# Optimization experiments

Hardware: AMD Instinct MI355X
Metric: run time of the kernel (lower is better)

The kernel has to match this reference:

```python
import jax, jax.numpy as jnp
import numpy as np

B, L, D, E, He = 8, 512, 300, 64, 64  # batch, seq_len, hidden_dim, edge_embed_dim, edge_hidden_dim


def setup_inputs() -> dict:
    key = jax.random.key(0)
    ks = jax.random.split(key, 7)
    return {
        "x": jax.random.normal(ks[0], (B, L, D), jnp.float32),
        "adj": jax.random.randint(ks[1], (B, L, L), 0, 2).astype(jnp.int32),
        "edge_embedding": jax.random.normal(ks[2], (B, L, L, E), jnp.float32),
        # learned params (xavier-ish scaling)
        "W_map": jax.random.normal(ks[3], (E, He), jnp.float32) / np.sqrt(E).astype(np.float32),
        "w_ew": jax.random.normal(ks[4], (He, 1), jnp.float32) / np.sqrt(He).astype(np.float32),
        "W_eto": jax.random.normal(ks[5], (D, D), jnp.float32) / np.sqrt(D).astype(np.float32),
        "b_eto": jnp.zeros((D,), jnp.float32),
    }


def reference(x, adj, edge_embedding, W_map, w_ew, W_eto, b_eto):
    # edge_mapping -> relu (dropout is identity in eval mode)
    em = jax.nn.relu(jnp.einsum('bije,eh->bijh', edge_embedding, W_map))  # [B,L,L,He]
    # edge_weight_liner (bias-free) -> [B,L,L]
    ew = jnp.einsum('bijh,ho->bij', em, w_ew)
    # row-wise abs-mean normalization (torch: mean(dim=-1).unsqueeze(-1), + 1e-10)
    row_mean = jnp.abs(jnp.mean(ew, axis=-1, keepdims=True)) + 1e-10
    ew = ew / row_mean
    # adjacency-masked softmax (torch uses -9e15 fill)
    scores = jnp.where(adj != 0, ew, jnp.float32(-9e15))
    att = jax.nn.softmax(scores, axis=-1)  # [B,L,L]
    # dense aggregation: edge_to(input) then attention matmul, relu
    h = x @ W_eto + b_eto  # [B,L,D]
    h_edge = jax.nn.relu(jnp.einsum('bij,bjd->bid', att, h))  # [B,L,D]
    return h_edge, att
```

## Files before the change

### kernel.cpp

```cpp
#include <hip/hip_runtime.h>
#include <hip/hip_bf16.h>

#define LSEQ 512
#define DDIM 300

typedef __attribute__((ext_vector_type(8))) short short8;
typedef __attribute__((ext_vector_type(4))) float f32x4;

__device__ __forceinline__ void split4(f32x4 v, short8& hi, short8& lo, int base) {
  #pragma unroll
  for (int e = 0; e < 4; ++e) {
    const float f = v[e];
    const unsigned b = __float_as_uint(f);
    const float hf = __uint_as_float(b & 0xffff0000u);
    hi[base + e] = (short)(b >> 16);
    lo[base + e] = (short)(__float_as_uint(f - hf) >> 16);
  }
}

__global__ __launch_bounds__(256, 3) void k_fused1(
    const float* __restrict__ emb, const int* __restrict__ adj,
    const float* __restrict__ Wmap, const float* __restrict__ wew,
    const float* __restrict__ x, const float* __restrict__ Weto,
    const float* __restrict__ beto,
    float* __restrict__ att, float* __restrict__ h) {
  __shared__ float stg[2][4][1024];
  __shared__ float ew_lds[LSEQ];
  __shared__ float redA[4], redB[4], redC[4];
  const int tid = threadIdx.x;
  const int lane = tid & 63, wid = tid >> 6;
  const int c = lane & 15, g = lane >> 4;

  if (blockIdx.x >= 4096) {
    const int gt = (blockIdx.x - 4096) * 4 + wid;
    const int rt = gt / 19, dt = gt % 19;
    const int r0 = rt * 16, d0 = dt * 16;
    const int dc = min(d0 + c, DDIM - 1);
    const float* xr = x + (size_t)(r0 + c) * DDIM;

    f32x4 acc = {0.f, 0.f, 0.f, 0.f};
    #pragma unroll 3
    for (int ks = 0; ks < 9; ++ks) {
      const int k0 = ks * 32 + 8 * g;
      const f32x4 a0 = *(const f32x4*)(xr + k0);
      const f32x4 a1 = *(const f32x4*)(xr + k0 + 4);
      short8 ahi, alo;
      split4(a0, ahi, alo, 0);
      split4(a1, ahi, alo, 4);
      const float* wp = Weto + (size_t)k0 * DDIM + dc;
      const f32x4 b0 = {wp[0], wp[DDIM], wp[2 * DDIM], wp[3 * DDIM]};
      const f32x4 b1 = {wp[4 * DDIM], wp[5 * DDIM], wp[6 * DDIM], wp[7 * DDIM]};
      short8 bhi, blo;
      split4(b0, bhi, blo, 0);
      split4(b1, bhi, blo, 4);
      acc = __builtin_amdgcn_mfma_f32_16x16x32_bf16(ahi, bhi, acc, 0, 0, 0);
      acc = __builtin_amdgcn_mfma_f32_16x16x32_bf16(ahi, blo, acc, 0, 0, 0);
      acc = __builtin_amdgcn_mfma_f32_16x16x32_bf16(alo, bhi, acc, 0, 0, 0);
    }
    {
      float av[8], bv[8];
      #pragma unroll
      for (int e = 0; e < 8; ++e) {
        const int kk = 288 + 8 * g + e;
        const bool ok = kk < DDIM;
        av[e] = ok ? xr[kk] : 0.f;
        bv[e] = ok ? Weto[(size_t)kk * DDIM + dc] : 0.f;
      }
      const f32x4 a0 = {av[0], av[1], av[2], av[3]};
      const f32x4 a1 = {av[4], av[5], av[6], av[7]};
      const f32x4 b0 = {bv[0], bv[1], bv[2], bv[3]};
      const f32x4 b1 = {bv[4], bv[5], bv[6], bv[7]};
      short8 ahi, alo, bhi, blo;
      split4(a0, ahi, alo, 0);
      split4(a1, ahi, alo, 4);
      split4(b0, bhi, blo, 0);
      split4(b1, bhi, blo, 4);
      acc = __builtin_amdgcn_mfma_f32_16x16x32_bf16(ahi, bhi, acc, 0, 0, 0);
      acc = __builtin_amdgcn_mfma_f32_16x16x32_bf16(ahi, blo, acc, 0, 0, 0);
      acc = __builtin_amdgcn_mfma_f32_16x16x32_bf16(alo, bhi, acc, 0, 0, 0);
    }
    if (d0 + c < DDIM) {
      const float bb = beto[d0 + c];
      #pragma unroll
      for (int reg = 0; reg < 4; ++reg)
        h[(size_t)(r0 + 4 * g + reg) * DDIM + d0 + c] = acc[reg] + bb;
    }
    return;
  }

  short8 whi[4][2], wlo[4][2];
  #pragma unroll
  for (int nt = 0; nt < 4; ++nt) {
    #pragma unroll
    for (int s = 0; s < 2; ++s) {
      #pragma unroll
      for (int e2 = 0; e2 < 2; ++e2) {
        f32x4 w;
        #pragma unroll
        for (int e = 0; e < 4; ++e)
          w[e] = Wmap[(32 * s + 8 * g + 4 * e2 + e) * 64 + 16 * nt + c];
        split4(w, whi[nt][s], wlo[nt][s], 4 * e2);
      }
    }
  }
  float wv2[4][4];
  #pragma unroll
  for (int nt = 0; nt < 4; ++nt)
    #pragma unroll
    for (int reg = 0; reg < 4; ++reg)
      wv2[nt][reg] = wew[16 * nt + 4 * g + reg];

  const size_t rowbase = (size_t)blockIdx.x * LSEQ;
  const size_t ebase = rowbase + (size_t)wid * 128;
  const float* gbase = emb + (ebase << 6);

  float* const lb0 = &stg[0][wid][0];
  float* const lb1 = &stg[1][wid][0];

  int wwb[4];
  #pragma unroll
  for (int i = 0; i < 4; ++i)
    wwb[i] = ((i * 1024 + lane * 16) ^ ((((i & 1) * 4 + g) & 7) << 4)) >> 2;

  const int rw0 = (c * 256 + (((2 * g + 0) ^ (c & 7)) << 4)) >> 2;
  const int rw1 = (c * 256 + (((2 * g + 1) ^ (c & 7)) << 4)) >> 2;
  const int rw2 = (c * 256 + (((2 * g + 8) ^ (c & 7)) << 4)) >> 2;
  const int rw3 = (c * 256 + (((2 * g + 9) ^ (c & 7)) << 4)) >> 2;

  f32x4 q0 = *(const f32x4*)(gbase + 0 * 256 + lane * 4);
  f32x4 q1 = *(const f32x4*)(gbase + 1 * 256 + lane * 4);
  f32x4 q2 = *(const f32x4*)(gbase + 2 * 256 + lane * 4);
  f32x4 q3 = *(const f32x4*)(gbase + 3 * 256 + lane * 4);
  *(f32x4*)(lb0 + wwb[0]) = q0;
  *(f32x4*)(lb0 + wwb[1]) = q1;
  *(f32x4*)(lb0 + wwb[2]) = q2;
  *(f32x4*)(lb0 + wwb[3]) = q3;

  #pragma unroll 1
  for (int it = 0; it < 8; ++it) {
    if (it < 7) {
      const float* nt_ = gbase + (size_t)(it + 1) * 1024;
      q0 = *(const f32x4*)(nt_ + 0 * 256 + lane * 4);
      q1 = *(const f32x4*)(nt_ + 1 * 256 + lane * 4);
      q2 = *(const f32x4*)(nt_ + 2 * 256 + lane * 4);
      q3 = *(const f32x4*)(nt_ + 3 * 256 + lane * 4);
    }
    float* const rb = (it & 1) ? lb1 : lb0;
    const f32x4 a0 = *(const f32x4*)(rb + rw0);
    const f32x4 a1 = *(const f32x4*)(rb + rw1);
    const f32x4 a2 = *(const f32x4*)(rb + rw2);
    const f32x4 a3 = *(const f32x4*)(rb + rw3);

    short8 ehi[2], elo[2];
    split4(a0, ehi[0], elo[0], 0);
    split4(a1, ehi[0], elo[0], 4);
    split4(a2, ehi[1], elo[1], 0);
    split4(a3, ehi[1], elo[1], 4);

    f32x4 acc[4];
    #pragma unroll
    for (int nt = 0; nt < 4; ++nt) acc[nt] = (f32x4){0.f, 0.f, 0.f, 0.f};
    #pragma unroll
    for (int s = 0; s < 2; ++s) {
      #pragma unroll
      for (int nt = 0; nt < 4; ++nt) {
        acc[nt] = __builtin_amdgcn_mfma_f32_16x16x32_bf16(whi[nt][s], ehi[s], acc[nt], 0, 0, 0);
        acc[nt] = __builtin_amdgcn_mfma_f32_16x16x32_bf16(whi[nt][s], elo[s], acc[nt], 0, 0, 0);
        acc[nt] = __builtin_amdgcn_mfma_f32_16x16x32_bf16(wlo[nt][s], ehi[s], acc[nt], 0, 0, 0);
      }
    }
    float p = 0.f;
    #pragma unroll
    for (int nt = 0; nt < 4; ++nt)
      #pragma unroll
      for (int reg = 0; reg < 4; ++reg)
        p = fmaf(fmaxf(acc[nt][reg], 0.f), wv2[nt][reg], p);
    p += __shfl_xor(p, 16, 64);
    p += __shfl_xor(p, 32, 64);
    if (lane < 16) ew_lds[wid * 128 + it * 16 + c] = p;

    if (it < 7) {
      float* const wb = (it & 1) ? lb0 : lb1;
      *(f32x4*)(wb + wwb[0]) = q0;
      *(f32x4*)(wb + wwb[1]) = q1;
      *(f32x4*)(wb + wwb[2]) = q2;
      *(f32x4*)(wb + wwb[3]) = q3;
    }
  }
  __syncthreads();

  const float ew0 = ew_lds[tid];
  const float ew1 = ew_lds[tid + 256];

  float ls = ew0 + ew1;
  #pragma unroll
  for (int m = 32; m >= 1; m >>= 1) ls += __shfl_xor(ls, m, 64);
  if (lane == 0) redA[wid] = ls;
  __syncthreads();
  const float rmean =
      fabsf((redA[0] + redA[1] + redA[2] + redA[3]) * (1.0f / 512.0f)) + 1e-10f;

  const int a0i = adj[rowbase + tid];
  const int a1i = adj[rowbase + tid + 256];
  const float sc0 = a0i ? (ew0 / rmean) : -9e15f;
  const float sc1 = a1i ? (ew1 / rmean) : -9e15f;

  float lm = fmaxf(sc0, sc1);
  #pragma unroll
  for (int m = 32; m >= 1; m >>= 1) lm = fmaxf(lm, __shfl_xor(lm, m, 64));
  if (lane == 0) redB[wid] = lm;
  __syncthreads();
  const float mx = fmaxf(fmaxf(redB[0], redB[1]), fmaxf(redB[2], redB[3]));

  const float e0 = expf(sc0 - mx);
  const float e1 = expf(sc1 - mx);
  float es = e0 + e1;
  #pragma unroll
  for (int m = 32; m >= 1; m >>= 1) es += __shfl_xor(es, m, 64);
  if (lane == 0) redC[wid] = es;
  __syncthreads();
  const float denom = redC[0] + redC[1] + redC[2] + redC[3];

  att[rowbase + tid] = e0 / denom;
  att[rowbase + tid + 256] = e1 / denom;
}

__global__ __launch_bounds__(256) void k_out(
    const float* __restrict__ att, const float* __restrict__ h,
    float* __restrict__ out) {
  const int tid = threadIdx.x;
  const int lane = tid & 63, wid = tid >> 6;
  const int c = lane & 15, g = lane >> 4;
  const int gt = blockIdx.x * 4 + wid;
  const int b = gt / 304, rem = gt % 304;
  const int i2 = rem / 19, dt = rem % 19;
  const int i0 = i2 * 32, d0 = dt * 16;
  const int dc = min(d0 + c, DDIM - 1);
  const float* attR0 = att + ((size_t)b * LSEQ + i0 + c) * LSEQ + 8 * g;
  const float* attR1 = attR0 + (size_t)16 * LSEQ;
  const float* hB = h + (size_t)b * LSEQ * DDIM;

  f32x4 acc0 = {0.f, 0.f, 0.f, 0.f};
  f32x4 acc1 = {0.f, 0.f, 0.f, 0.f};
  #pragma unroll 2
  for (int ks = 0; ks < 16; ++ks) {
    const int k0 = ks * 32;
    const f32x4 a0 = *(const f32x4*)(attR0 + k0);
    const f32x4 a1 = *(const f32x4*)(attR0 + k0 + 4);
    const f32x4 a2 = *(const f32x4*)(attR1 + k0);
    const f32x4 a3 = *(const f32x4*)(attR1 + k0 + 4);
    short8 ahi0, alo0, ahi1, alo1;
    split4(a0, ahi0, alo0, 0);
    split4(a1, ahi0, alo0, 4);
    split4(a2, ahi1, alo1, 0);
    split4(a3, ahi1, alo1, 4);
    const float* hp = hB + (size_t)(k0 + 8 * g) * DDIM + dc;
    const f32x4 b0 = {hp[0], hp[DDIM], hp[2 * DDIM], hp[3 * DDIM]};
    const f32x4 b1 = {hp[4 * DDIM], hp[5 * DDIM], hp[6 * DDIM], hp[7 * DDIM]};
    short8 bhi, blo;
    split4(b0, bhi, blo, 0);
    split4(b1, bhi, blo, 4);
    acc0 = __builtin_amdgcn_mfma_f32_16x16x32_bf16(ahi0, bhi, acc0, 0, 0, 0);
    acc0 = __builtin_amdgcn_mfma_f32_16x16x32_bf16(ahi0, blo, acc0, 0, 0, 0);
    acc0 = __builtin_amdgcn_mfma_f32_16x16x32_bf16(alo0, bhi, acc0, 0, 0, 0);
    acc1 = __builtin_amdgcn_mfma_f32_16x16x32_bf16(ahi1, bhi, acc1, 0, 0, 0);
    acc1 = __builtin_amdgcn_mfma_f32_16x16x32_bf16(ahi1, blo, acc1, 0, 0, 0);
    acc1 = __builtin_amdgcn_mfma_f32_16x16x32_bf16(alo1, bhi, acc1, 0, 0, 0);
  }
  if (d0 + c < DDIM) {
    #pragma unroll
    for (int reg = 0; reg < 4; ++reg) {
      out[((size_t)b * LSEQ + i0 + 4 * g + reg) * DDIM + d0 + c] =
          fmaxf(acc0[reg], 0.f);
      out[((size_t)b * LSEQ + i0 + 16 + 4 * g + reg) * DDIM + d0 + c] =
          fmaxf(acc1[reg], 0.f);
    }
  }
}

extern "C" void kernel_launch(void* const* d_in, const int* in_sizes, int n_in,
                              void* d_out, int out_size, void* d_ws, size_t ws_size,
                              hipStream_t stream) {
  const float* x    = (const float*)d_in[0];
  const int*   adj  = (const int*)d_in[1];
  const float* emb  = (const float*)d_in[2];
  const float* Wmap = (const float*)d_in[3];
  const float* wew  = (const float*)d_in[4];
  const float* Weto = (const float*)d_in[5];
  const float* beto = (const float*)d_in[6];

  float* out    = (float*)d_out;
  float* h_edge = out;
  float* att    = out + (size_t)8 * LSEQ * DDIM;
  float* h      = (float*)d_ws;

  k_fused1<<<dim3(4096 + 1216), 256, 0, stream>>>(emb, adj, Wmap, wew, x, Weto,
                                                  beto, att, h);
  k_out<<<dim3(608), 256, 0, stream>>>(att, h, h_edge);
}
```

Baseline: 145.5 us.

## Store h transposed and pre-split into packed bf16 hi/lo for k_out

The projection stage now writes h as a transposed [B, D_pad, L] array of packed bf16 hi/lo pairs instead of row-major fp32. k_out can then load its B operand with contiguous 16-byte vector loads and skip the per-iteration fp32-to-bf16 split. The goal is to replace the strided scalar gathers across rows of h and to avoid repeating the split work that every attention tile did before. In exchange, the h writes in the first kernel become strided across d, and padded columns are stored as zeros.

```diff
diff --git a/kernel.cpp b/kernel.cpp
--- a/kernel.cpp
+++ b/kernel.cpp
@@ -3,9 +3,11 @@
 
 #define LSEQ 512
 #define DDIM 300
+#define DPAD 304
 
 typedef __attribute__((ext_vector_type(8))) short short8;
 typedef __attribute__((ext_vector_type(4))) float f32x4;
+typedef __attribute__((ext_vector_type(4))) unsigned u32x4;
 
 __device__ __forceinline__ void split4(f32x4 v, short8& hi, short8& lo, int base) {
   #pragma unroll
@@ -18,12 +20,20 @@
   }
 }
 
+__device__ __forceinline__ unsigned pack_split(float f) {
+  const unsigned b = __float_as_uint(f);
+  const float hf = __uint_as_float(b & 0xffff0000u);
+  const unsigned hi = b >> 16;
+  const unsigned lo = __float_as_uint(f - hf) >> 16;
+  return (hi & 0xffffu) | (lo << 16);
+}
+
 __global__ __launch_bounds__(256, 3) void k_fused1(
     const float* __restrict__ emb, const int* __restrict__ adj,
     const float* __restrict__ Wmap, const float* __restrict__ wew,
     const float* __restrict__ x, const float* __restrict__ Weto,
     const float* __restrict__ beto,
-    float* __restrict__ att, float* __restrict__ h) {
+    float* __restrict__ att, unsigned* __restrict__ hs) {
   __shared__ float stg[2][4][1024];
   __shared__ float ew_lds[LSEQ];
   __shared__ float redA[4], redB[4], redC[4];
@@ -79,12 +89,15 @@
       acc = __builtin_amdgcn_mfma_f32_16x16x32_bf16(ahi, blo, acc, 0, 0, 0);
       acc = __builtin_amdgcn_mfma_f32_16x16x32_bf16(alo, bhi, acc, 0, 0, 0);
     }
-    if (d0 + c < DDIM) {
-      const float bb = beto[d0 + c];
-      #pragma unroll
-      for (int reg = 0; reg < 4; ++reg)
-        h[(size_t)(r0 + 4 * g + reg) * DDIM + d0 + c] = acc[reg] + bb;
-    }
+    const int bidx = r0 >> 9;
+    const int il0 = (r0 & 511) + 4 * g;
+    const bool valid = (d0 + c) < DDIM;
+    const float bb = valid ? beto[d0 + c] : 0.f;
+    u32x4 pk;
+    #pragma unroll
+    for (int reg = 0; reg < 4; ++reg)
+      pk[reg] = valid ? pack_split(acc[reg] + bb) : 0u;
+    *(u32x4*)(hs + ((size_t)bidx * DPAD + d0 + c) * LSEQ + il0) = pk;
     return;
   }
 
@@ -226,19 +239,18 @@
 }
 
 __global__ __launch_bounds__(256) void k_out(
-    const float* __restrict__ att, const float* __restrict__ h,
+    const float* __restrict__ att, const unsigned* __restrict__ hs,
     float* __restrict__ out) {
   const int tid = threadIdx.x;
   const int lane = tid & 63, wid = tid >> 6;
-  const int c = lane & 15, g = lane >> 4;
+  const int c = lane & 15, gg = lane >> 4;
   const int gt = blockIdx.x * 4 + wid;
   const int b = gt / 304, rem = gt % 304;
   const int i2 = rem / 19, dt = rem % 19;
   const int i0 = i2 * 32, d0 = dt * 16;
-  const int dc = min(d0 + c, DDIM - 1);
-  const float* attR0 = att + ((size_t)b * LSEQ + i0 + c) * LSEQ + 8 * g;
+  const float* attR0 = att + ((size_t)b * LSEQ + i0 + c) * LSEQ + 8 * gg;
   const float* attR1 = attR0 + (size_t)16 * LSEQ;
-  const float* hB = h + (size_t)b * LSEQ * DDIM;
+  const unsigned* hsp = hs + ((size_t)b * DPAD + d0 + c) * LSEQ;
 
   f32x4 acc0 = {0.f, 0.f, 0.f, 0.f};
   f32x4 acc1 = {0.f, 0.f, 0.f, 0.f};
@@ -254,12 +266,16 @@
     split4(a1, ahi0, alo0, 4);
     split4(a2, ahi1, alo1, 0);
     split4(a3, ahi1, alo1, 4);
-    const float* hp = hB + (size_t)(k0 + 8 * g) * DDIM + dc;
-    const f32x4 b0 = {hp[0], hp[DDIM], hp[2 * DDIM], hp[3 * DDIM]};
-    const f32x4 b1 = {hp[4 * DDIM], hp[5 * DDIM], hp[6 * DDIM], hp[7 * DDIM]};
+    const u32x4 u0 = *(const u32x4*)(hsp + k0 + 8 * gg);
+    const u32x4 u1 = *(const u32x4*)(hsp + k0 + 8 * gg + 4);
     short8 bhi, blo;
-    split4(b0, bhi, blo, 0);
-    split4(b1, bhi, blo, 4);
+    #pragma unroll
+    for (int e = 0; e < 4; ++e) {
+      bhi[e] = (short)(u0[e] & 0xffffu);
+      blo[e] = (short)(u0[e] >> 16);
+      bhi[4 + e] = (short)(u1[e] & 0xffffu);
+      blo[4 + e] = (short)(u1[e] >> 16);
+    }
     acc0 = __builtin_amdgcn_mfma_f32_16x16x32_bf16(ahi0, bhi, acc0, 0, 0, 0);
     acc0 = __builtin_amdgcn_mfma_f32_16x16x32_bf16(ahi0, blo, acc0, 0, 0, 0);
     acc0 = __builtin_amdgcn_mfma_f32_16x16x32_bf16(alo0, bhi, acc0, 0, 0, 0);
@@ -270,9 +286,9 @@
   if (d0 + c < DDIM) {
     #pragma unroll
     for (int reg = 0; reg < 4; ++reg) {
-      out[((size_t)b * LSEQ + i0 + 4 * g + reg) * DDIM + d0 + c] =
+      out[((size_t)b * LSEQ + i0 + 4 * gg + reg) * DDIM + d0 + c] =
           fmaxf(acc0[reg], 0.f);
-      out[((size_t)b * LSEQ + i0 + 16 + 4 * g + reg) * DDIM + d0 + c] =
+      out[((size_t)b * LSEQ + i0 + 16 + 4 * gg + reg) * DDIM + d0 + c] =
           fmaxf(acc1[reg], 0.f);
     }
   }
@@ -289,12 +305,12 @@
   const float* Weto = (const float*)d_in[5];
   const float* beto = (const float*)d_in[6];
 
-  float* out    = (float*)d_out;
-  float* h_edge = out;
-  float* att    = out + (size_t)8 * LSEQ * DDIM;
-  float* h      = (float*)d_ws;
+  float* out      = (float*)d_out;
+  float* h_edge   = out;
+  float* att      = out + (size_t)8 * LSEQ * DDIM;
+  unsigned* hs    = (unsigned*)d_ws;
 
   k_fused1<<<dim3(4096 + 1216), 256, 0, stream>>>(emb, adj, Wmap, wew, x, Weto,
-                                                  beto, att, h);
-  k_out<<<dim3(608), 256, 0, stream>>>(att, h, h_edge);
-}
+                                                  beto, att, hs);
+  k_out<<<dim3(608), 256, 0, stream>>>(att, hs, h_edge);
+}
```

Measured after the change: 152.2 us. 4.6% more time.

## Stage h tiles in double-buffered LDS and widen k_out blocks over all columns

Applied to the files above, without the earlier changes.

The attention-times-h kernel now gives each block 16 query rows across all 300 output columns. It streams 32-row tiles of h through a double-buffered shared-memory buffer, so the attention rows are read once per block rather than once per column tile. The h workspace is padded to a 304-float row stride so tiles can be loaded with aligned vector loads. The trade-offs are a large LDS footprint and only one 256-block wave of work. The prefetch is also synchronous global-to-LDS copying, which may stall the waves.

```diff
diff --git a/kernel.cpp b/kernel.cpp
--- a/kernel.cpp
+++ b/kernel.cpp
@@ -3,6 +3,7 @@
 
 #define LSEQ 512
 #define DDIM 300
+#define HPAD 304
 
 typedef __attribute__((ext_vector_type(8))) short short8;
 typedef __attribute__((ext_vector_type(4))) float f32x4;
@@ -83,7 +84,7 @@
       const float bb = beto[d0 + c];
       #pragma unroll
       for (int reg = 0; reg < 4; ++reg)
-        h[(size_t)(r0 + 4 * g + reg) * DDIM + d0 + c] = acc[reg] + bb;
+        h[(size_t)(r0 + 4 * g + reg) * HPAD + d0 + c] = acc[reg] + bb;
     }
     return;
   }
@@ -228,52 +229,79 @@
 __global__ __launch_bounds__(256) void k_out(
     const float* __restrict__ att, const float* __restrict__ h,
     float* __restrict__ out) {
+  __shared__ float lds_h[2][32 * HPAD];
   const int tid = threadIdx.x;
   const int lane = tid & 63, wid = tid >> 6;
   const int c = lane & 15, g = lane >> 4;
-  const int gt = blockIdx.x * 4 + wid;
-  const int b = gt / 304, rem = gt % 304;
-  const int i2 = rem / 19, dt = rem % 19;
-  const int i0 = i2 * 32, d0 = dt * 16;
-  const int dc = min(d0 + c, DDIM - 1);
-  const float* attR0 = att + ((size_t)b * LSEQ + i0 + c) * LSEQ + 8 * g;
-  const float* attR1 = attR0 + (size_t)16 * LSEQ;
-  const float* hB = h + (size_t)b * LSEQ * DDIM;
-
-  f32x4 acc0 = {0.f, 0.f, 0.f, 0.f};
-  f32x4 acc1 = {0.f, 0.f, 0.f, 0.f};
-  #pragma unroll 2
+  const int b = blockIdx.x & 7;
+  const int i0 = (blockIdx.x >> 3) * 16;
+  const float* hB = h + (size_t)b * LSEQ * HPAD;
+  const float* attR = att + ((size_t)b * LSEQ + i0 + c) * LSEQ + 8 * g;
+
+  f32x4 acc[5];
+  #pragma unroll
+  for (int j = 0; j < 5; ++j) acc[j] = (f32x4){0.f, 0.f, 0.f, 0.f};
+
+  #pragma unroll
+  for (int j = 0; j < 10; ++j) {
+    const int v = tid + 256 * j;
+    if (v < 2432)
+      *(f32x4*)(&lds_h[0][4 * v]) = *(const f32x4*)(hB + 4 * v);
+  }
+  __syncthreads();
+
+  #pragma unroll 1
   for (int ks = 0; ks < 16; ++ks) {
-    const int k0 = ks * 32;
-    const f32x4 a0 = *(const f32x4*)(attR0 + k0);
-    const f32x4 a1 = *(const f32x4*)(attR0 + k0 + 4);
-    const f32x4 a2 = *(const f32x4*)(attR1 + k0);
-    const f32x4 a3 = *(const f32x4*)(attR1 + k0 + 4);
-    short8 ahi0, alo0, ahi1, alo1;
-    split4(a0, ahi0, alo0, 0);
-    split4(a1, ahi0, alo0, 4);
-    split4(a2, ahi1, alo1, 0);
-    split4(a3, ahi1, alo1, 4);
-    const float* hp = hB + (size_t)(k0 + 8 * g) * DDIM + dc;
-    const f32x4 b0 = {hp[0], hp[DDIM], hp[2 * DDIM], hp[3 * DDIM]};
-    const f32x4 b1 = {hp[4 * DDIM], hp[5 * DDIM], hp[6 * DDIM], hp[7 * DDIM]};
-    short8 bhi, blo;
-    split4(b0, bhi, blo, 0);
-    split4(b1, bhi, blo, 4);
-    acc0 = __builtin_amdgcn_mfma_f32_16x16x32_bf16(ahi0, bhi, acc0, 0, 0, 0);
-    acc0 = __builtin_amdgcn_mfma_f32_16x16x32_bf16(ahi0, blo, acc0, 0, 0, 0);
-    acc0 = __builtin_amdgcn_mfma_f32_16x16x32_bf16(alo0, bhi, acc0, 0, 0, 0);
-    acc1 = __builtin_amdgcn_mfma_f32_16x16x32_bf16(ahi1, bhi, acc1, 0, 0, 0);
-    acc1 = __builtin_amdgcn_mfma_f32_16x16x32_bf16(ahi1, blo, acc1, 0, 0, 0);
-    acc1 = __builtin_amdgcn_mfma_f32_16x16x32_bf16(alo1, bhi, acc1, 0, 0, 0);
-  }
-  if (d0 + c < DDIM) {
-    #pragma unroll
-    for (int reg = 0; reg < 4; ++reg) {
-      out[((size_t)b * LSEQ + i0 + 4 * g + reg) * DDIM + d0 + c] =
-          fmaxf(acc0[reg], 0.f);
-      out[((size_t)b * LSEQ + i0 + 16 + 4 * g + reg) * DDIM + d0 + c] =
-          fmaxf(acc1[reg], 0.f);
+    const float* cur = lds_h[ks & 1];
+    if (ks < 15) {
+      float* nxt = lds_h[(ks + 1) & 1];
+      const float* src = hB + (size_t)(ks + 1) * 32 * HPAD;
+      #pragma unroll
+      for (int j = 0; j < 10; ++j) {
+        const int v = tid + 256 * j;
+        if (v < 2432)
+          *(f32x4*)(&nxt[4 * v]) = *(const f32x4*)(src + 4 * v);
+      }
+    }
+    const f32x4 a0 = *(const f32x4*)(attR + ks * 32);
+    const f32x4 a1 = *(const f32x4*)(attR + ks * 32 + 4);
+    short8 ahi, alo;
+    split4(a0, ahi, alo, 0);
+    split4(a1, ahi, alo, 4);
+    const int krow = 8 * g;
+    #pragma unroll
+    for (int j = 0; j < 5; ++j) {
+      const int dt = wid + 4 * j;
+      if (dt < 19) {
+        const int d = dt * 16 + c;
+        f32x4 b0, b1;
+        #pragma unroll
+        for (int e = 0; e < 4; ++e) {
+          b0[e] = cur[(krow + e) * HPAD + d];
+          b1[e] = cur[(krow + 4 + e) * HPAD + d];
+        }
+        short8 bhi, blo;
+        split4(b0, bhi, blo, 0);
+        split4(b1, bhi, blo, 4);
+        acc[j] = __builtin_amdgcn_mfma_f32_16x16x32_bf16(ahi, bhi, acc[j], 0, 0, 0);
+        acc[j] = __builtin_amdgcn_mfma_f32_16x16x32_bf16(ahi, blo, acc[j], 0, 0, 0);
+        acc[j] = __builtin_amdgcn_mfma_f32_16x16x32_bf16(alo, bhi, acc[j], 0, 0, 0);
+      }
+    }
+    __syncthreads();
+  }
+
+  #pragma unroll
+  for (int j = 0; j < 5; ++j) {
+    const int dt = wid + 4 * j;
+    if (dt < 19) {
+      const int d = dt * 16 + c;
+      if (d < DDIM) {
+        #pragma unroll
+        for (int reg = 0; reg < 4; ++reg)
+          out[((size_t)b * LSEQ + i0 + 4 * g + reg) * DDIM + d] =
+              fmaxf(acc[j][reg], 0.f);
+      }
     }
   }
 }
@@ -296,5 +324,5 @@
 
   k_fused1<<<dim3(4096 + 1216), 256, 0, stream>>>(emb, adj, Wmap, wew, x, Weto,
                                                   beto, att, h);
-  k_out<<<dim3(608), 256, 0, stream>>>(att, h, h_edge);
+  k_out<<<dim3(256), 256, 0, stream>>>(att, h, h_edge);
 }
```

Result: slower. 159.3 us (+9.5%).
